# Optimization experiments

Measured on AMD Instinct MI355X. Metric: run time of the kernel, lower is better.

The kernel has to match this reference:

```python
import jax, jax.numpy as jnp
import numpy as np


def get_rel_pos(q_size, k_size, rel_pos):
    # table length == 2*max(q,k)-1, so no interpolation branch is needed.
    # relative coords: i - j + (k_size - 1) (q_size == k_size here)
    coords = jnp.arange(q_size)[:, None] - jnp.arange(k_size)[None, :] + (k_size - 1)
    return rel_pos[coords]  # (q_size, k_size, head_dim)


def setup_inputs() -> dict:
    key = jax.random.key(0)
    ks = jax.random.split(key, 11)
    B, H, W, C = 4, 32, 32, 768
    nH, d = 12, 64
    L = 2 * H - 1
    s = 0.02
    return {
        "x": jax.random.normal(ks[0], (B, H, W, C), jnp.float32),
        "Wq": jax.random.normal(ks[1], (nH, d, C), jnp.float32) * s,
        "Wk": jax.random.normal(ks[2], (nH, d, C), jnp.float32) * s,
        "Wv": jax.random.normal(ks[3], (nH, d, C), jnp.float32) * s,
        "bq": jax.random.normal(ks[4], (nH, d), jnp.float32) * s,
        "bk": jax.random.normal(ks[5], (nH, d), jnp.float32) * s,
        "bv": jax.random.normal(ks[6], (nH, d), jnp.float32) * s,
        "rel_pos_h": jax.random.normal(ks[7], (L, d), jnp.float32) * s,
        "rel_pos_w": jax.random.normal(ks[8], (L, d), jnp.float32) * s,
        "proj_w": jax.random.normal(ks[9], (C, C), jnp.float32) * s,
        "proj_b": jax.random.normal(ks[10], (C,), jnp.float32) * s,
    }


def reference(x, Wq, Wk, Wv, bq, bk, bv, rel_pos_h, rel_pos_w, proj_w, proj_b):
    B, H, W, C = x.shape
    nH, d, _ = Wq.shape
    scale = d ** -0.5
    S = H * W

    # Per-head 1x1-conv QKV projection (split-head loop in the original ==
    # one batched einsum over the head axis; same math).
    q = jnp.einsum('bhwc,ndc->bnhwd', x, Wq) + bq[None, :, None, None, :]
    k = jnp.einsum('bhwc,ndc->bnhwd', x, Wk) + bk[None, :, None, None, :]
    v = jnp.einsum('bhwc,ndc->bnhwd', x, Wv) + bv[None, :, None, None, :]

    qf = q.reshape(B, nH, S, d)
    kf = k.reshape(B, nH, S, d)
    vf = v.reshape(B, nH, S, d)

    # (q * scale) @ k^T -> (B, nH, S, S)
    attn = jnp.einsum('bnqd,bnkd->bnqk', qf * scale, kf)

    # Decomposed relative position bias
    Rh = get_rel_pos(H, H, rel_pos_h)  # (H, H, d)
    Rw = get_rel_pos(W, W, rel_pos_w)  # (W, W, d)
    rel_h = jnp.einsum('bnhwd,hkd->bnhwk', q, Rh)  # (B, nH, H, W, k_h)
    rel_w = jnp.einsum('bnhwd,wkd->bnhwk', q, Rw)  # (B, nH, H, W, k_w)
    attn = (attn.reshape(B, nH, H, W, H, W)
            + rel_h[:, :, :, :, :, None]
            + rel_w[:, :, :, :, None, :]).reshape(B, nH, S, S)

    attn = jax.nn.softmax(attn, axis=-1)
    out = jnp.einsum('bnqk,bnkd->bnqd', attn, vf)  # (B, nH, S, d)
    # concat heads: (B, nH, H, W, d) -> (B, H, W, nH*d)
    out = out.reshape(B, nH, H, W, d).transpose(0, 2, 3, 1, 4).reshape(B, H, W, nH * d)
    # output projection (1x1 conv == linear)
    return out @ proj_w.T + proj_b
```

## Files before the change

### kernel.cpp

```cpp
#include <hip/hip_runtime.h>
#include <hip/hip_bf16.h>
#include <math.h>

typedef float4 f4;
typedef __attribute__((ext_vector_type(8))) short bf16x8;
typedef __attribute__((ext_vector_type(4))) float f32x4;
typedef __attribute__((ext_vector_type(16))) float f32x16;

#define CD   768
#define SEQ  1024
#define NHD  12
#define DH   64

__device__ __forceinline__ ushort f2bf(float x) {
    union { __hip_bfloat16 h; ushort u; } v;
    v.h = __float2bfloat16(x);
    return v.u;
}
__device__ __forceinline__ unsigned pk2bf(float a, float b) {
    union { __hip_bfloat162 h; unsigned u; } v;
    v.h = __float22bfloat162_rn(make_float2(a, b));
    return v.u;
}
__device__ __forceinline__ void gload_lds16(const ushort* g, ushort* l) {
    __builtin_amdgcn_global_load_lds((const __attribute__((address_space(1))) void*)g,
                                     (__attribute__((address_space(3))) void*)l, 16, 0, 0);
}

__global__ __launch_bounds__(256) void cvt_bf16_k(
    const float* __restrict__ x, const float* __restrict__ Wq,
    const float* __restrict__ Wk, const float* __restrict__ Wv,
    const float* __restrict__ pw, ushort* __restrict__ dst)
{
    const int idx = blockIdx.x * 256 + threadIdx.x;
    if (idx >= 1376256) return;
    const int e = idx << 2;
    if (e < 4915200) {
        const float* src; int off;
        if      (e < 3145728) { src = x;  off = e; }
        else if (e < 3735552) { src = Wq; off = e - 3145728; }
        else if (e < 4325376) { src = Wk; off = e - 3735552; }
        else                  { src = Wv; off = e - 4325376; }
        const f4 v = *(const f4*)(src + off);
        uint2 o;
        o.x = pk2bf(v.x, v.y);
        o.y = pk2bf(v.z, v.w);
        *(uint2*)(dst + e) = o;
    } else {
        const int off = e - 4915200;
        const int n = off / CD, k = off - n * CD;
        const f4 v = *(const f4*)(pw + off);
        uint2 o;
        o.x = pk2bf(v.x, v.y);
        o.y = pk2bf(v.z, v.w);
        *(uint2*)(dst + 4915200 + ((size_t)(k >> 6) * CD + n) * 64 + (k & 63)) = o;
    }
}

__global__ __launch_bounds__(256, 2) void qkv_mfma(
    const ushort* __restrict__ xbf,
    const ushort* __restrict__ wq, const ushort* __restrict__ wk, const ushort* __restrict__ wv,
    const float* __restrict__ bq, const float* __restrict__ bk, const float* __restrict__ bv,
    ushort* __restrict__ qbf, ushort* __restrict__ kbf, ushort* __restrict__ vbfT)
{
    __shared__ __align__(16) ushort Sq[28672];

    const int t = threadIdx.x;
    const int w = t >> 6, l = t & 63;
    const int lr = l & 15, lg = l >> 4;
    const int n0 = blockIdx.x * 96;
    const int m0 = blockIdx.y << 7;
    const int sel  = n0 / CD;
    const int nloc = n0 % CD;
    const ushort* Wb  = (sel == 0) ? wq : ((sel == 1) ? wk : wv);
    const float* bias = (sel == 0) ? bq : ((sel == 1) ? bk : bv);

    const int srow = (w << 3) + (l >> 3);
    const int scol = (l & 7) << 3;
    const ushort* Agl = xbf + (size_t)(m0 + srow) * CD + scol;
    const ushort* Bgl = Wb + (size_t)(nloc + srow) * CD + scol;

    f32x4 acc[4][3];
    #pragma unroll
    for (int mi = 0; mi < 4; ++mi)
        #pragma unroll
        for (int ni = 0; ni < 3; ++ni) acc[mi][ni] = (f32x4){0.f, 0.f, 0.f, 0.f};

    const int mb = (w >> 1) << 6;
    const int nb = (w & 1) * 48;

    #pragma unroll
    for (int i = 0; i < 4; ++i)
        gload_lds16(Agl + (size_t)(i << 5) * CD, &Sq[(i << 11) + (w << 9)]);
    #pragma unroll
    for (int i = 0; i < 3; ++i)
        gload_lds16(Bgl + (size_t)(i << 5) * CD, &Sq[8192 + (i << 11) + (w << 9)]);
    __syncthreads();

    for (int kt = 0; kt < 12; ++kt) {
        const int cb = (kt & 1) * 14336;
        if (kt < 11) {
            const int nbuf = ((kt + 1) & 1) * 14336;
            const int kc = (kt + 1) << 6;
            #pragma unroll
            for (int i = 0; i < 4; ++i)
                gload_lds16(Agl + (size_t)(i << 5) * CD + kc, &Sq[nbuf + (i << 11) + (w << 9)]);
            #pragma unroll
            for (int i = 0; i < 3; ++i)
                gload_lds16(Bgl + (size_t)(i << 5) * CD + kc, &Sq[nbuf + 8192 + (i << 11) + (w << 9)]);
        }
        #pragma unroll
        for (int kk = 0; kk < 2; ++kk) {
            bf16x8 af[4], bf[3];
            #pragma unroll
            for (int mi = 0; mi < 4; ++mi)
                af[mi] = *(const bf16x8*)&Sq[cb + (mb + (mi << 4) + lr) * 64 + (kk << 5) + (lg << 3)];
            #pragma unroll
            for (int ni = 0; ni < 3; ++ni)
                bf[ni] = *(const bf16x8*)&Sq[cb + 8192 + (nb + (ni << 4) + lr) * 64 + (kk << 5) + (lg << 3)];
            #pragma unroll
            for (int mi = 0; mi < 4; ++mi)
                #pragma unroll
                for (int ni = 0; ni < 3; ++ni)
                    acc[mi][ni] = __builtin_amdgcn_mfma_f32_16x16x32_bf16(af[mi], bf[ni], acc[mi][ni], 0, 0, 0);
        }
        __syncthreads();
    }

    ushort* Ep = Sq + w * 3072;

    float bl[3];
    #pragma unroll
    for (int ni = 0; ni < 3; ++ni) bl[ni] = bias[nloc + nb + (ni << 4) + lr];

    if (sel < 2) {
        #pragma unroll
        for (int mi = 0; mi < 4; ++mi)
            #pragma unroll
            for (int ni = 0; ni < 3; ++ni)
                #pragma unroll
                for (int reg = 0; reg < 4; ++reg)
                    Ep[((mi << 4) + (lg << 2) + reg) * 48 + (ni << 4) + lr] =
                        f2bf(acc[mi][ni][reg] + bl[ni]);
    } else {
        #pragma unroll
        for (int mi = 0; mi < 4; ++mi)
            #pragma unroll
            for (int ni = 0; ni < 3; ++ni)
                #pragma unroll
                for (int reg = 0; reg < 4; ++reg)
                    Ep[((ni << 4) + lr) * 64 + (lg << 4) + (reg << 2) + mi] =
                        f2bf(acc[mi][ni][reg] + bl[ni]);
    }
    __syncthreads();

    const int bi  = m0 >> 10;
    const int si0 = (m0 & 1023) + mb;
    if (sel < 2) {
        ushort* dbf = (sel == 0) ? qbf : kbf;
        #pragma unroll
        for (int i = 0; i < 6; ++i) {
            const int c0   = i << 3;
            const int head = (nloc + nb + c0) >> 6;
            const int dd0  = (nloc + nb + c0) & 63;
            const int bn   = bi * NHD + head;
            *(bf16x8*)(dbf + (((size_t)bn << 10) + si0 + l) * 64 + dd0) =
                *(const bf16x8*)(Ep + l * 48 + c0);
        }
    } else {
        #pragma unroll
        for (int i = 0; i < 6; ++i) {
            const int idx = (i << 6) + l;
            const int r   = idx >> 3, ch = idx & 7;
            const int head = (nloc + nb + r) >> 6;
            const int d    = (nloc + nb + r) & 63;
            const int bn   = bi * NHD + head;
            *(bf16x8*)(vbfT + (((size_t)(bn * DH + d)) << 10) + si0 + (ch << 3)) =
                *(const bf16x8*)(Ep + r * 64 + (ch << 3));
        }
    }
}

__global__ __launch_bounds__(256, 3) void attn_mfma(
    const ushort* __restrict__ qbf, const ushort* __restrict__ kbf,
    const ushort* __restrict__ vbfT,
    const float* __restrict__ rph, const float* __restrict__ rpw,
    ushort* __restrict__ abf2)
{
    __shared__ __align__(16) ushort KV[2][8192];
    __shared__ __align__(16) ushort Pl[4][16][72];
    __shared__ __align__(16) float rhs_[2048];

    const int t  = threadIdx.x;
    const int l  = t & 63, w = t >> 6;
    const int lr = l & 15, lg = l >> 4;
    const int qt = blockIdx.x, bn = blockIdx.y;
    const int q0 = qt << 6;

    {
        const int p   = w >> 1;
        const int sub = w & 1;
        const int h   = (qt << 1) + p;
        const int q5  = l & 31, g = l >> 5;

        const ushort* qp = qbf + (((size_t)bn << 10) + (h << 5) + q5) * 64 + (g << 3);
        bf16x8 qf[4];
        #pragma unroll
        for (int c = 0; c < 4; ++c) qf[c] = *(const bf16x8*)(qp + (c << 4));

        float* PwF = (float*)&KV[0][0] + p * 2112;

        if (sub == 0) {
            f32x16 acch;
            #pragma unroll
            for (int i = 0; i < 16; ++i) acch[i] = 0.f;
            {
                const float* rp = rph + (size_t)(h + 31 - q5) * 64 + (g << 3);
                #pragma unroll
                for (int c = 0; c < 4; ++c) {
                    const f4 v0 = *(const f4*)(rp + (c << 4));
                    const f4 v1 = *(const f4*)(rp + (c << 4) + 4);
                    union { unsigned u[4]; bf16x8 v; } u;
                    u.u[0] = pk2bf(v0.x, v0.y); u.u[1] = pk2bf(v0.z, v0.w);
                    u.u[2] = pk2bf(v1.x, v1.y); u.u[3] = pk2bf(v1.z, v1.w);
                    acch = __builtin_amdgcn_mfma_f32_32x32x16_bf16(u.v, qf[c], acch, 0, 0, 0);
                }
            }
            #pragma unroll
            for (int r = 0; r < 16; r += 2) {
                const int k2 = (r & 3) + ((r >> 2) << 3) + (g << 2);
                *(float2*)&rhs_[((k2 >> 1) << 7) + (((p << 5) + q5) << 1)] =
                    make_float2(acch[r], acch[r + 1]);
            }
            f32x16 accw;
            #pragma unroll
            for (int i = 0; i < 16; ++i) accw[i] = 0.f;
            {
                const float* rp = rpw + (size_t)q5 * 64 + (g << 3);
                #pragma unroll
                for (int c = 0; c < 4; ++c) {
                    const f4 v0 = *(const f4*)(rp + (c << 4));
                    const f4 v1 = *(const f4*)(rp + (c << 4) + 4);
                    union { unsigned u[4]; bf16x8 v; } u;
                    u.u[0] = pk2bf(v0.x, v0.y); u.u[1] = pk2bf(v0.z, v0.w);
                    u.u[2] = pk2bf(v1.x, v1.y); u.u[3] = pk2bf(v1.z, v1.w);
                    accw = __builtin_amdgcn_mfma_f32_32x32x16_bf16(u.v, qf[c], accw, 0, 0, 0);
                }
            }
            #pragma unroll
            for (int r = 0; r < 16; ++r) {
                const int row = (r & 3) + ((r >> 2) << 3) + (g << 2);
                PwF[row * 33 + q5] = accw[r];
            }
        } else {
            f32x16 accw;
            #pragma unroll
            for (int i = 0; i < 16; ++i) accw[i] = 0.f;
            {
                const bool ok = (32 + q5) < 63;
                const float* rp = rpw + (size_t)(32 + q5) * 64 + (g << 3);
                #pragma unroll
                for (int c = 0; c < 4; ++c) {
                    union { unsigned u[4]; bf16x8 v; } u;
                    if (ok) {
                        const f4 v0 = *(const f4*)(rp + (c << 4));
                        const f4 v1 = *(const f4*)(rp + (c << 4) + 4);
                        u.u[0] = pk2bf(v0.x, v0.y); u.u[1] = pk2bf(v0.z, v0.w);
                        u.u[2] = pk2bf(v1.x, v1.y); u.u[3] = pk2bf(v1.z, v1.w);
                    } else {
                        u.u[0] = 0u; u.u[1] = 0u; u.u[2] = 0u; u.u[3] = 0u;
                    }
                    accw = __builtin_amdgcn_mfma_f32_32x32x16_bf16(u.v, qf[c], accw, 0, 0, 0);
                }
            }
            #pragma unroll
            for (int r = 0; r < 16; ++r) {
                const int row = (r & 3) + ((r >> 2) << 3) + (g << 2) + 32;
                PwF[row * 33 + q5] = accw[r];
            }
        }
    }
    __syncthreads();

    float rw_[4][2];
    {
        const int p = w >> 1;
        const float* PwF = (float*)&KV[0][0] + p * 2112;
        #pragma unroll
        for (int reg = 0; reg < 4; ++reg) {
            const int q5w = ((w & 1) << 4) + (lg << 2) + reg;
            rw_[reg][0] = PwF[(q5w + 31 - lr) * 33 + q5w];
            rw_[reg][1] = PwF[(q5w + 15 - lr) * 33 + q5w];
        }
    }
    __syncthreads();

    const ushort* qp = qbf + (((size_t)bn << 10) + q0 + w * 16 + lr) * DH + lg * 8;
    const bf16x8 qa0 = *(const bf16x8*)qp;
    const bf16x8 qa1 = *(const bf16x8*)(qp + 32);

    const int rhbase = ((w * 16 + lg * 4) << 1);

    const int i0   = w << 1;
    const int rsub = l >> 3;
    const int coff = ((l & 7) ^ rsub) << 3;
    const size_t kbase = ((size_t)bn << 16);
    const ushort* kp0 = kbf + kbase + (size_t)((i0 << 3) + rsub) * 64 + coff;
    const ushort* kp1 = kp0 + 512;
    const ushort* vp0 = vbfT + kbase + ((size_t)((i0 << 3) + rsub) << 10) + coff;
    const ushort* vp1 = vp0 + 8192;
    const int lds0 = i0 << 9;

    f32x4 oc[4];
    #pragma unroll
    for (int nf = 0; nf < 4; ++nf) oc[nf] = (f32x4){0.f, 0.f, 0.f, 0.f};
    f32x4 sumc = (f32x4){0.f, 0.f, 0.f, 0.f};
    bf16x8 ones;
    #pragma unroll
    for (int i = 0; i < 8; ++i) ones[i] = (short)0x3F80;

    const int s0c = lg ^ (lr & 7);

    gload_lds16(kp0, &KV[0][lds0]);
    gload_lds16(kp1, &KV[0][lds0 + 512]);
    gload_lds16(vp0, &KV[0][4096 + lds0]);
    gload_lds16(vp1, &KV[0][4096 + lds0 + 512]);
    __syncthreads();

    for (int kt = 0; kt < 16; ++kt) {
        const int cur = kt & 1;
        if (kt < 15) {
            ushort* nb_ = &KV[cur ^ 1][0];
            gload_lds16(kp0 + ((kt + 1) << 12), nb_ + lds0);
            gload_lds16(kp1 + ((kt + 1) << 12), nb_ + lds0 + 512);
            gload_lds16(vp0 + ((kt + 1) << 6), nb_ + 4096 + lds0);
            gload_lds16(vp1 + ((kt + 1) << 6), nb_ + 4096 + lds0 + 512);
        }
        const ushort* Kl = &KV[cur][0];
        const ushort* Vt = &KV[cur][4096];
        const f4 rh01 = *(const f4*)&rhs_[(kt << 7) + rhbase];
        const f4 rh23 = *(const f4*)&rhs_[(kt << 7) + rhbase + 4];

        f32x4 sc[4];
        #pragma unroll
        for (int f = 0; f < 4; ++f) {
            f32x4 c = (f32x4){0.f, 0.f, 0.f, 0.f};
            const int rb = (f * 16 + lr) * 64;
            const bf16x8 kb0 = *(const bf16x8*)&Kl[rb + (s0c << 3)];
            const bf16x8 kb1 = *(const bf16x8*)&Kl[rb + ((s0c ^ 4) << 3)];
            c = __builtin_amdgcn_mfma_f32_16x16x32_bf16(qa0, kb0, c, 0, 0, 0);
            c = __builtin_amdgcn_mfma_f32_16x16x32_bf16(qa1, kb1, c, 0, 0, 0);
            sc[f] = c;
        }

        #pragma unroll
        for (int reg = 0; reg < 4; ++reg) {
            const float rhx = (reg == 0) ? rh01.x : (reg == 1) ? rh01.z
                             : (reg == 2) ? rh23.x : rh23.z;
            const float rhy = (reg == 0) ? rh01.y : (reg == 1) ? rh01.w
                             : (reg == 2) ? rh23.y : rh23.w;
            const float e0 = __expf(fmaf(sc[0][reg], 0.125f, rhx + rw_[reg][0]));
            const float e1 = __expf(fmaf(sc[1][reg], 0.125f, rhx + rw_[reg][1]));
            const float e2 = __expf(fmaf(sc[2][reg], 0.125f, rhy + rw_[reg][0]));
            const float e3 = __expf(fmaf(sc[3][reg], 0.125f, rhy + rw_[reg][1]));
            uint2 pk;
            pk.x = pk2bf(e0, e1);
            pk.y = pk2bf(e2, e3);
            *(uint2*)&Pl[w][lg * 4 + reg][lr * 4] = pk;
        }

        const bf16x8 pa0 = *(const bf16x8*)&Pl[w][lr][lg * 8];
        const bf16x8 pa1 = *(const bf16x8*)&Pl[w][lr][lg * 8 + 32];
        sumc = __builtin_amdgcn_mfma_f32_16x16x32_bf16(pa0, ones, sumc, 0, 0, 0);
        sumc = __builtin_amdgcn_mfma_f32_16x16x32_bf16(pa1, ones, sumc, 0, 0, 0);
        #pragma unroll
        for (int nf = 0; nf < 4; ++nf) {
            const int rb = (nf * 16 + lr) * 64;
            const bf16x8 vb0 = *(const bf16x8*)&Vt[rb + (s0c << 3)];
            const bf16x8 vb1 = *(const bf16x8*)&Vt[rb + ((s0c ^ 4) << 3)];
            oc[nf] = __builtin_amdgcn_mfma_f32_16x16x32_bf16(pa0, vb0, oc[nf], 0, 0, 0);
            oc[nf] = __builtin_amdgcn_mfma_f32_16x16x32_bf16(pa1, vb1, oc[nf], 0, 0, 0);
        }
        __syncthreads();
    }

    const int bi = bn / NHD, hn = bn - bi * NHD;
    #pragma unroll
    for (int reg = 0; reg < 4; ++reg) {
        const float inv = 1.f / sumc[reg];
        const int row = q0 + w * 16 + lg * 4 + reg;
        ushort* dst = abf2 + ((size_t)hn * 4096 + (bi << 10) + row) * 64 + lr;
        union { unsigned u; ushort2 s2; } a, b;
        a.u = pk2bf(oc[0][reg] * inv, oc[1][reg] * inv);
        b.u = pk2bf(oc[2][reg] * inv, oc[3][reg] * inv);
        dst[0]  = a.s2.x;
        dst[16] = a.s2.y;
        dst[32] = b.s2.x;
        dst[48] = b.s2.y;
    }
}

__global__ __launch_bounds__(256, 2) void proj_mfma(
    const ushort* __restrict__ abf2, const ushort* __restrict__ pwbf2,
    const float* __restrict__ pb, float* __restrict__ out)
{
    __shared__ __align__(16) ushort Sp[20480];

    const int t = threadIdx.x;
    const int w = t >> 6, l = t & 63;
    const int lr = l & 15, lg = l >> 4;
    const int n0 = blockIdx.x * 96;
    const int m0 = blockIdx.y << 6;

    const int srow = l >> 3;
    const int scol = (l & 7) << 3;
    const ushort* Agl = abf2 + (size_t)(m0 + (w << 4) + srow) * 64 + scol;
    const ushort* Bgl = pwbf2 + (size_t)(n0 + w * 24 + srow) * 64 + scol;

    f32x4 acc[2][3];
    #pragma unroll
    for (int mi = 0; mi < 2; ++mi)
        #pragma unroll
        for (int ni = 0; ni < 3; ++ni) acc[mi][ni] = (f32x4){0.f, 0.f, 0.f, 0.f};

    const int mb = (w >> 1) << 5;
    const int nb = (w & 1) * 48;

    #pragma unroll
    for (int i = 0; i < 2; ++i)
        gload_lds16(Agl + (i << 9), &Sp[(w << 10) + (i << 9)]);
    #pragma unroll
    for (int j = 0; j < 3; ++j)
        gload_lds16(Bgl + (j << 9), &Sp[4096 + w * 1536 + (j << 9)]);
    __syncthreads();

    for (int kt = 0; kt < 12; ++kt) {
        const int cb = (kt & 1) * 10240;
        if (kt < 11) {
            const int nbuf = ((kt + 1) & 1) * 10240;
            const size_t pA = (size_t)(kt + 1) * 262144;
            const size_t pB = (size_t)(kt + 1) * 49152;
            #pragma unroll
            for (int i = 0; i < 2; ++i)
                gload_lds16(Agl + pA + (i << 9), &Sp[nbuf + (w << 10) + (i << 9)]);
            #pragma unroll
            for (int j = 0; j < 3; ++j)
                gload_lds16(Bgl + pB + (j << 9), &Sp[nbuf + 4096 + w * 1536 + (j << 9)]);
        }
        #pragma unroll
        for (int kk = 0; kk < 2; ++kk) {
            bf16x8 af[2], bf[3];
            #pragma unroll
            for (int mi = 0; mi < 2; ++mi)
                af[mi] = *(const bf16x8*)&Sp[cb + (mb + (mi << 4) + lr) * 64 + (kk << 5) + (lg << 3)];
            #pragma unroll
            for (int ni = 0; ni < 3; ++ni)
                bf[ni] = *(const bf16x8*)&Sp[cb + 4096 + (nb + (ni << 4) + lr) * 64 + (kk << 5) + (lg << 3)];
            #pragma unroll
            for (int mi = 0; mi < 2; ++mi)
                #pragma unroll
                for (int ni = 0; ni < 3; ++ni)
                    acc[mi][ni] = __builtin_amdgcn_mfma_f32_16x16x32_bf16(af[mi], bf[ni], acc[mi][ni], 0, 0, 0);
        }
        __syncthreads();
    }

    float bl[3];
    #pragma unroll
    for (int ni = 0; ni < 3; ++ni) bl[ni] = pb[n0 + nb + (ni << 4) + lr];
    #pragma unroll
    for (int mi = 0; mi < 2; ++mi)
        #pragma unroll
        for (int ni = 0; ni < 3; ++ni)
            #pragma unroll
            for (int reg = 0; reg < 4; ++reg)
                out[(size_t)(m0 + mb + (mi << 4) + (lg << 2) + reg) * CD
                    + n0 + nb + (ni << 4) + lr] = acc[mi][ni][reg] + bl[ni];
}

extern "C" void kernel_launch(void* const* d_in, const int* in_sizes, int n_in,
                              void* d_out, int out_size, void* d_ws, size_t ws_size,
                              hipStream_t stream) {
    (void)in_sizes; (void)n_in; (void)out_size; (void)ws_size;
    const float* x   = (const float*)d_in[0];
    const float* Wq  = (const float*)d_in[1];
    const float* Wk  = (const float*)d_in[2];
    const float* Wv  = (const float*)d_in[3];
    const float* bq  = (const float*)d_in[4];
    const float* bk  = (const float*)d_in[5];
    const float* bv  = (const float*)d_in[6];
    const float* rph = (const float*)d_in[7];
    const float* rpw = (const float*)d_in[8];
    const float* pw  = (const float*)d_in[9];
    const float* pb  = (const float*)d_in[10];
    float* out = (float*)d_out;

    ushort* cvt  = (ushort*)d_ws;
    ushort* xbf  = cvt;
    ushort* wqbf = cvt + 3145728;
    ushort* wkbf = wqbf + 589824;
    ushort* wvbf = wkbf + 589824;
    ushort* pwbf = wvbf + 589824;
    ushort* qbf  = pwbf + 589824;
    ushort* kbf  = qbf  + 3145728;
    ushort* vbfT = kbf  + 3145728;
    ushort* abf2 = vbfT + 3145728;

    hipLaunchKernelGGL(cvt_bf16_k, dim3(5376), dim3(256), 0, stream,
                       x, Wq, Wk, Wv, pw, cvt);
    hipLaunchKernelGGL(qkv_mfma, dim3(24, 32), dim3(256), 0, stream,
                       xbf, wqbf, wkbf, wvbf, bq, bk, bv, qbf, kbf, vbfT);
    hipLaunchKernelGGL(attn_mfma, dim3(16, 48), dim3(256), 0, stream,
                       qbf, kbf, vbfT, rph, rpw, abf2);
    hipLaunchKernelGGL(proj_mfma, dim3(8, 64), dim3(256), 0, stream,
                       abf2, pwbf, pb, out);
}
```

Measured before the change: 81.06 us.

## Keep softmax probabilities in registers by transposing QK^T MFMA operands

Swaps the A/B operands of the QK^T MFMA so each lane holds scores for one query row across keys, which lets the exponentiated probabilities be packed directly into the PV MFMA A-operand registers. This removes the per-tile LDS round trip through the Pl buffer (store, then reload). The V-transpose epilogue layout and the rel-pos bias register mapping are permuted to match the new key ordering. The risk is a wrong key permutation between P and V, plus some extra register pressure.

```diff
diff --git a/kernel.cpp b/kernel.cpp
--- a/kernel.cpp
+++ b/kernel.cpp
@@ -21,6 +21,11 @@
     union { __hip_bfloat162 h; unsigned u; } v;
     v.h = __float22bfloat162_rn(make_float2(a, b));
     return v.u;
+}
+__device__ __forceinline__ bf16x8 mk_bf16x8(unsigned a, unsigned b, unsigned c, unsigned d) {
+    union { unsigned u[4]; bf16x8 v; } r;
+    r.u[0] = a; r.u[1] = b; r.u[2] = c; r.u[3] = d;
+    return r.v;
 }
 __device__ __forceinline__ void gload_lds16(const ushort* g, ushort* l) {
     __builtin_amdgcn_global_load_lds((const __attribute__((address_space(1))) void*)g,
@@ -149,7 +154,8 @@
             for (int ni = 0; ni < 3; ++ni)
                 #pragma unroll
                 for (int reg = 0; reg < 4; ++reg)
-                    Ep[((ni << 4) + lr) * 64 + (lg << 4) + (reg << 2) + mi] =
+                    Ep[((ni << 4) + lr) * 64 +
+                       ((mi >> 1) << 5) + (lg << 3) + ((mi & 1) << 2) + reg] =
                         f2bf(acc[mi][ni][reg] + bl[ni]);
     }
     __syncthreads();
@@ -188,7 +194,6 @@
     ushort* __restrict__ abf2)
 {
     __shared__ __align__(16) ushort KV[2][8192];
-    __shared__ __align__(16) ushort Pl[4][16][72];
     __shared__ __align__(16) float rhs_[2048];
 
     const int t  = threadIdx.x;
@@ -282,16 +287,18 @@
     }
     __syncthreads();
 
-    float rw_[4][2];
+    float rw8[8];
     {
-        const int p = w >> 1;
+        const int p   = w >> 1;
+        const int q5w = ((w & 1) << 4) + lr;
         const float* PwF = (float*)&KV[0][0] + p * 2112;
         #pragma unroll
-        for (int reg = 0; reg < 4; ++reg) {
-            const int q5w = ((w & 1) << 4) + (lg << 2) + reg;
-            rw_[reg][0] = PwF[(q5w + 31 - lr) * 33 + q5w];
-            rw_[reg][1] = PwF[(q5w + 15 - lr) * 33 + q5w];
-        }
+        for (int b = 0; b < 2; ++b)
+            #pragma unroll
+            for (int reg = 0; reg < 4; ++reg) {
+                const int k2 = (b << 4) + (lg << 2) + reg;
+                rw8[(b << 2) + reg] = PwF[(q5w + 31 - k2) * 33 + q5w];
+            }
     }
     __syncthreads();
 
@@ -299,7 +306,7 @@
     const bf16x8 qa0 = *(const bf16x8*)qp;
     const bf16x8 qa1 = *(const bf16x8*)(qp + 32);
 
-    const int rhbase = ((w * 16 + lg * 4) << 1);
+    const int rhbase = (w * 16 + lr) << 1;
 
     const int i0   = w << 1;
     const int rsub = l >> 3;
@@ -338,8 +345,7 @@
         }
         const ushort* Kl = &KV[cur][0];
         const ushort* Vt = &KV[cur][4096];
-        const f4 rh01 = *(const f4*)&rhs_[(kt << 7) + rhbase];
-        const f4 rh23 = *(const f4*)&rhs_[(kt << 7) + rhbase + 4];
+        const float2 rh = *(const float2*)&rhs_[(kt << 7) + rhbase];
 
         f32x4 sc[4];
         #pragma unroll
@@ -348,29 +354,27 @@
             const int rb = (f * 16 + lr) * 64;
             const bf16x8 kb0 = *(const bf16x8*)&Kl[rb + (s0c << 3)];
             const bf16x8 kb1 = *(const bf16x8*)&Kl[rb + ((s0c ^ 4) << 3)];
-            c = __builtin_amdgcn_mfma_f32_16x16x32_bf16(qa0, kb0, c, 0, 0, 0);
-            c = __builtin_amdgcn_mfma_f32_16x16x32_bf16(qa1, kb1, c, 0, 0, 0);
+            c = __builtin_amdgcn_mfma_f32_16x16x32_bf16(kb0, qa0, c, 0, 0, 0);
+            c = __builtin_amdgcn_mfma_f32_16x16x32_bf16(kb1, qa1, c, 0, 0, 0);
             sc[f] = c;
         }
 
-        #pragma unroll
-        for (int reg = 0; reg < 4; ++reg) {
-            const float rhx = (reg == 0) ? rh01.x : (reg == 1) ? rh01.z
-                             : (reg == 2) ? rh23.x : rh23.z;
-            const float rhy = (reg == 0) ? rh01.y : (reg == 1) ? rh01.w
-                             : (reg == 2) ? rh23.y : rh23.w;
-            const float e0 = __expf(fmaf(sc[0][reg], 0.125f, rhx + rw_[reg][0]));
-            const float e1 = __expf(fmaf(sc[1][reg], 0.125f, rhx + rw_[reg][1]));
-            const float e2 = __expf(fmaf(sc[2][reg], 0.125f, rhy + rw_[reg][0]));
-            const float e3 = __expf(fmaf(sc[3][reg], 0.125f, rhy + rw_[reg][1]));
-            uint2 pk;
-            pk.x = pk2bf(e0, e1);
-            pk.y = pk2bf(e2, e3);
-            *(uint2*)&Pl[w][lg * 4 + reg][lr * 4] = pk;
-        }
-
-        const bf16x8 pa0 = *(const bf16x8*)&Pl[w][lr][lg * 8];
-        const bf16x8 pa1 = *(const bf16x8*)&Pl[w][lr][lg * 8 + 32];
+        unsigned ua[4], ub[4];
+        #pragma unroll
+        for (int f = 0; f < 4; ++f) {
+            const float rhv = (f & 2) ? rh.y : rh.x;
+            const int rb8 = (f & 1) << 2;
+            const float e0 = __expf(fmaf(sc[f][0], 0.125f, rhv + rw8[rb8 + 0]));
+            const float e1 = __expf(fmaf(sc[f][1], 0.125f, rhv + rw8[rb8 + 1]));
+            const float e2 = __expf(fmaf(sc[f][2], 0.125f, rhv + rw8[rb8 + 2]));
+            const float e3 = __expf(fmaf(sc[f][3], 0.125f, rhv + rw8[rb8 + 3]));
+            unsigned* du = (f & 2) ? ub : ua;
+            du[((f & 1) << 1) + 0] = pk2bf(e0, e1);
+            du[((f & 1) << 1) + 1] = pk2bf(e2, e3);
+        }
+        const bf16x8 pa0 = mk_bf16x8(ua[0], ua[1], ua[2], ua[3]);
+        const bf16x8 pa1 = mk_bf16x8(ub[0], ub[1], ub[2], ub[3]);
+
         sumc = __builtin_amdgcn_mfma_f32_16x16x32_bf16(pa0, ones, sumc, 0, 0, 0);
         sumc = __builtin_amdgcn_mfma_f32_16x16x32_bf16(pa1, ones, sumc, 0, 0, 0);
         #pragma unroll
```

New measurement: 79.61 us. Within noise of the previous version (-1.8%).
